# Performance work log

Hardware: AMD Instinct MI355X
Metric: run time of the kernel (lower is better)

The kernel has to match this reference:

```python
import jax, jax.numpy as jnp
import numpy as np

N = 50000          # num nodes
E = 800000         # num edges
DIN = 128          # in_channels
C = 64             # out_channels per head
H = 2              # heads
ED = 32            # edge_dim


def setup_inputs() -> dict:
    key = jax.random.key(0)
    ks = jax.random.split(key, 12)
    s = 1.0 / np.sqrt(DIN)
    se = 1.0 / np.sqrt(ED)
    return {
        "x": jax.random.normal(ks[0], (N, DIN), dtype=jnp.float32),
        "edge_index": jax.random.randint(ks[1], (2, E), 0, N, dtype=jnp.int32),
        "edge_attr": jax.random.normal(ks[2], (E, ED), dtype=jnp.float32),
        "Wq": jax.random.uniform(ks[3], (DIN, H * C), jnp.float32, -s, s),
        "bq": jax.random.uniform(ks[4], (H * C,), jnp.float32, -s, s),
        "Wk": jax.random.uniform(ks[5], (DIN, H * C), jnp.float32, -s, s),
        "bk": jax.random.uniform(ks[6], (H * C,), jnp.float32, -s, s),
        "Wv": jax.random.uniform(ks[7], (DIN, H * C), jnp.float32, -s, s),
        "bv": jax.random.uniform(ks[8], (H * C,), jnp.float32, -s, s),
        "We": jax.random.uniform(ks[9], (ED, H * C), jnp.float32, -se, se),
        "Wskip": jax.random.uniform(ks[10], (DIN, H * C), jnp.float32, -s, s),
        "bskip": jax.random.uniform(ks[11], (H * C,), jnp.float32, -s, s),
    }


def reference(x, edge_index, edge_attr, Wq, bq, Wk, bk, Wv, bv, We, Wskip, bskip):
    src, dst = edge_index[0], edge_index[1]
    # node-level projections [N, H, C]
    q = (x @ Wq + bq).reshape(N, H, C)
    k = (x @ Wk + bk).reshape(N, H, C)
    v = (x @ Wv + bv).reshape(N, H, C)
    e = (edge_attr @ We).reshape(E, H, C)  # lin_edge, no bias

    # per-edge gather
    q_e = q[dst]              # [E, H, C]
    k_e = k[src] + e          # key gets edge features
    alpha = jnp.einsum("ehc,ehc->eh", q_e, k_e) / jnp.sqrt(jnp.float32(C))

    # segment softmax over incoming edges of each dst node
    m = jax.ops.segment_max(alpha, dst, num_segments=N)       # [N, H]
    alpha = jnp.exp(alpha - m[dst])
    denom = jax.ops.segment_sum(alpha, dst, num_segments=N)   # [N, H]
    alpha = alpha / (denom[dst] + 1e-16)

    # weighted aggregation of values (value also gets edge features)
    msg = (v[src] + e) * alpha[..., None]                     # [E, H, C]
    out = jax.ops.segment_sum(msg, dst, num_segments=N)       # [N, H, C]
    out = out.reshape(N, H * C)

    # root weight skip connection (concat=True, beta=False)
    return out + x @ Wskip + bskip
```

## Files before the change

### kernel.cpp

```cpp
#include <hip/hip_runtime.h>
#include <cstdint>

#define NN 50000
#define EE 800000
#define DINC 128
#define HC 128
#define EDC 32
#define CAP 64
#define GEMM_BLKS 3128
#define SCAT_BLKS 3125
#define NB_SCAN 196

typedef __attribute__((ext_vector_type(8))) short short8;
typedef __attribute__((ext_vector_type(4))) float floatx4;

__device__ __forceinline__ unsigned int pk2(float a, float b){
  unsigned int ua = __float_as_uint(a), ub = __float_as_uint(b);
  ua = (ua + 0x7FFFu + ((ua >> 16) & 1u)) >> 16;
  ub = (ub + 0x7FFFu + ((ub >> 16) & 1u)) & 0xFFFF0000u;
  return ua | ub;
}
__device__ __forceinline__ float bflo(unsigned int p){ return __uint_as_float(p << 16); }
__device__ __forceinline__ float bfhi(unsigned int p){ return __uint_as_float(p & 0xFFFF0000u); }

__global__ __launch_bounds__(256) void k_fused(
    const float* __restrict__ x,
    const float* __restrict__ Wq, const float* __restrict__ bq,
    const float* __restrict__ Wk, const float* __restrict__ bk,
    const float* __restrict__ Wv, const float* __restrict__ bv,
    const float* __restrict__ Wsk, const float* __restrict__ bsk,
    const int* __restrict__ ei,
    unsigned int* __restrict__ qbf, unsigned int* __restrict__ kv,
    float* __restrict__ out, int* __restrict__ cnt, int2* __restrict__ eidsrc,
    const int do_scatter)
{
  __shared__ unsigned int smem[64*68 + 128*68];

  if (do_scatter && blockIdx.x >= GEMM_BLKS){
    int e = (blockIdx.x - GEMM_BLKS)*256 + threadIdx.x;
    if (e < EE){
      int d = ei[EE + e];
      int s = ei[e];
      int pos = atomicAdd(cnt + d, 1);
      if (pos < CAP) eidsrc[(size_t)d*CAP + pos] = make_int2(e, s);
    }
    return;
  }

  unsigned int* sx = smem;
  unsigned int* sw = smem + 64*68;
  float* facc = (float*)sw;

  const int tid = threadIdx.x;
  const int mat = blockIdx.x & 3;
  const int bm  = (blockIdx.x >> 2) * 64;
  const float* W  = (mat==0)?Wq:(mat==1)?Wk:(mat==2)?Wv:Wsk;
  const float* bi = (mat==0)?bq:(mat==1)?bk:(mat==2)?bv:bsk;

  for (int idx = tid; idx < 64*64; idx += 256){
    int row = idx >> 6, kk = idx & 63;
    int gr = bm + row;
    unsigned int p = 0u;
    if (gr < NN){
      float2 v = *(const float2*)(x + (size_t)gr*DINC + 2*kk);
      p = pk2(v.x, v.y);
    }
    sx[row*68 + kk] = p;
  }
  for (int idx = tid; idx < 64*64; idx += 256){
    int kp = idx >> 6;
    int n2 = (idx & 63) * 2;
    float2 a = *(const float2*)(W + (2*kp)*HC + n2);
    float2 b = *(const float2*)(W + (2*kp+1)*HC + n2);
    sw[n2*68 + kp]     = pk2(a.x, b.x);
    sw[(n2+1)*68 + kp] = pk2(a.y, b.y);
  }
  __syncthreads();

  const int l = tid & 63, wid = tid >> 6;
  const int lm = l & 15, ks = l >> 4;
  const int n0 = wid * 32;

  floatx4 acc[4][2];
  #pragma unroll
  for (int mt=0;mt<4;mt++) for(int nt=0;nt<2;nt++) acc[mt][nt] = (floatx4){0.f,0.f,0.f,0.f};

  #pragma unroll
  for (int kb = 0; kb < 4; ++kb){
    short8 a[4], b[2];
    #pragma unroll
    for (int mt=0;mt<4;mt++)
      a[mt] = *(const short8*)(sx + (mt*16+lm)*68 + kb*16 + ks*4);
    #pragma unroll
    for (int nt=0;nt<2;nt++)
      b[nt] = *(const short8*)(sw + (n0+nt*16+lm)*68 + kb*16 + ks*4);
    #pragma unroll
    for (int mt=0;mt<4;mt++)
      #pragma unroll
      for (int nt=0;nt<2;nt++)
        acc[mt][nt] = __builtin_amdgcn_mfma_f32_16x16x32_bf16(a[mt], b[nt], acc[mt][nt], 0, 0, 0);
  }
  __syncthreads();

  #pragma unroll
  for (int mt=0;mt<4;mt++)
    #pragma unroll
    for (int nt=0;nt<2;nt++)
      #pragma unroll
      for (int r=0;r<4;r++){
        int row = mt*16 + ks*4 + r;
        int col = n0 + nt*16 + lm;
        facc[row*132 + col] = acc[mt][nt][r];
      }
  __syncthreads();

  for (int idx = tid; idx < 64*64; idx += 256){
    int row = idx >> 6, cp = idx & 63;
    int gr = bm + row;
    if (gr >= NN) continue;
    float v0 = facc[row*132 + 2*cp]     + bi[2*cp];
    float v1 = facc[row*132 + 2*cp + 1] + bi[2*cp+1];
    if (mat == 0)      qbf[gr*64 + cp] = pk2(v0, v1);
    else if (mat == 1) kv[(size_t)gr*128 + 2*cp]     = pk2(v0, v1);
    else if (mat == 2) kv[(size_t)gr*128 + 2*cp + 1] = pk2(v0, v1);
    else *(float2*)(out + (size_t)gr*HC + 2*cp) = make_float2(v0, v1);
  }
}

__global__ __launch_bounds__(256) void k_count(const int* __restrict__ ei,
    int* __restrict__ cnt)
{
  int e = blockIdx.x*256 + threadIdx.x;
  if (e < EE) atomicAdd(cnt + ei[EE + e], 1);
}
__global__ __launch_bounds__(256) void k_blksum(const int* __restrict__ cnt,
    int* __restrict__ bsum)
{
  __shared__ int s[256];
  int t = threadIdx.x, i = blockIdx.x*256 + t;
  s[t] = (i < NN) ? cnt[i] : 0;
  __syncthreads();
  for (int d = 128; d > 0; d >>= 1){
    if (t < d) s[t] += s[t + d];
    __syncthreads();
  }
  if (t == 0) bsum[blockIdx.x] = s[0];
}
__global__ __launch_bounds__(256) void k_bscan(const int* __restrict__ bsum,
    int* __restrict__ bpre)
{
  __shared__ int s[256];
  int t = threadIdx.x;
  int v = (t < NB_SCAN) ? bsum[t] : 0;
  s[t] = v;
  __syncthreads();
  for (int d = 1; d < 256; d <<= 1){
    int u = (t >= d) ? s[t - d] : 0;
    __syncthreads();
    s[t] += u;
    __syncthreads();
  }
  if (t < NB_SCAN) bpre[t] = s[t] - v;
}
__global__ __launch_bounds__(256) void k_scan3(const int* __restrict__ cnt,
    const int* __restrict__ bpre, int* __restrict__ off, int* __restrict__ woff)
{
  __shared__ int s[256];
  int t = threadIdx.x, i = blockIdx.x*256 + t;
  int v = (i < NN) ? cnt[i] : 0;
  s[t] = v;
  __syncthreads();
  for (int d = 1; d < 256; d <<= 1){
    int u = (t >= d) ? s[t - d] : 0;
    __syncthreads();
    s[t] += u;
    __syncthreads();
  }
  if (i < NN){
    int o = bpre[blockIdx.x] + s[t] - v;
    off[i] = o; woff[i] = o;
  }
}
__global__ __launch_bounds__(256) void k_scatter(const int* __restrict__ ei,
    int* __restrict__ woff, int2* __restrict__ eidsrc)
{
  int e = blockIdx.x*256 + threadIdx.x;
  if (e < EE){
    int d = ei[EE + e];
    int s = ei[e];
    int pos = atomicAdd(woff + d, 1);
    eidsrc[pos] = make_int2(e, s);
  }
}

__global__ __launch_bounds__(256) void k_agg(
    const float* __restrict__ eattr, const float* __restrict__ We,
    const unsigned int* __restrict__ qbf, const uint2* __restrict__ kv,
    const int* __restrict__ cnt, const int* __restrict__ off,
    const int2* __restrict__ eidsrc, const int fixed,
    float* __restrict__ out)
{
  __shared__ float sWeT[128*33];
  const int tid = threadIdx.x;
  for (int idx = tid; idx < EDC*HC; idx += 256){
    int jj = idx >> 7, col = idx & 127;
    sWeT[col*33 + jj] = We[idx];
  }
  __syncthreads();

  const int wid = tid >> 6, l = tid & 63;
  const int node = blockIdx.x*4 + wid;
  const int h = l >> 5, j = l & 31;

  int deg = cnt[node]; if (deg > CAP) deg = CAP;
  const size_t beg = fixed ? (size_t)node*CAP : (size_t)off[node];
  int2 esl = eidsrc[beg + (fixed ? l : (l < deg ? l : 0))];

  unsigned int qp = qbf[node*64 + l];
  float q0 = bflo(qp), q1 = bfhi(qp);
  float Pl = 0.f;
  {
    const unsigned int* qrow = qbf + node*64 + h*32;
    const float* wt = sWeT + (h*64)*33 + j;
    #pragma unroll 8
    for (int cc = 0; cc < 32; ++cc){
      unsigned int up = qrow[cc];
      Pl += bflo(up)*wt[(2*cc)*33] + bfhi(up)*wt[(2*cc+1)*33];
    }
  }

  float acc0=0.f, acc1=0.f, wea=0.f, den=0.f;
  if (deg > 0){
    float eav[4]; uint2 kx[4];
    #pragma unroll
    for (int t = 0; t < 4; ++t){
      int it  = (t < deg) ? t : 0;
      int eid = __shfl(esl.x, it, 64);
      int src = __shfl(esl.y, it, 64);
      eav[t] = eattr[(size_t)eid*EDC + j];
      kx[t]  = kv[(size_t)src*64 + l];
    }
    for (int i = 0; i < deg; i += 4){
      float eavn[4]; uint2 kxn[4];
      const int inext = i + 4;
      if (inext < deg){
        #pragma unroll
        for (int t = 0; t < 4; ++t){
          int it  = (inext + t < deg) ? inext + t : inext;
          int eid = __shfl(esl.x, it, 64);
          int src = __shfl(esl.y, it, 64);
          eavn[t] = eattr[(size_t)eid*EDC + j];
          kxn[t]  = kv[(size_t)src*64 + l];
        }
      }
      float p[4];
      #pragma unroll
      for (int t = 0; t < 4; ++t)
        p[t] = q0*bflo(kx[t].x) + q1*bfhi(kx[t].x) + Pl*eav[t];
      #pragma unroll
      for (int s = 1; s < 32; s <<= 1){
        #pragma unroll
        for (int t = 0; t < 4; ++t) p[t] += __shfl_xor(p[t], s, 32);
      }
      const int nb = deg - i;
      #pragma unroll
      for (int t = 0; t < 4; ++t){
        float a = __expf(p[t] * 0.125f);
        if (t > 0) a = (t < nb) ? a : 0.f;
        den  += a;
        acc0 += a*bflo(kx[t].y);
        acc1 += a*bfhi(kx[t].y);
        wea  += a*eav[t];
      }
      #pragma unroll
      for (int t = 0; t < 4; ++t){ eav[t] = eavn[t]; kx[t] = kxn[t]; }
    }
  }

  float rden = 1.0f/(den + 1e-16f);
  float e0 = 0.f, e1 = 0.f;
  const float* w0 = sWeT + (2*l)*33;
  const float* w1 = sWeT + (2*l+1)*33;
  #pragma unroll 8
  for (int jj = 0; jj < 32; ++jj){
    float w = __shfl(wea, h*32 + jj, 64);
    e0 += w*w0[jj]; e1 += w*w1[jj];
  }
  float2 sk = *(const float2*)(out + (size_t)node*HC + 2*l);
  float2 o;
  o.x = sk.x + (acc0 + e0)*rden;
  o.y = sk.y + (acc1 + e1)*rden;
  *(float2*)(out + (size_t)node*HC + 2*l) = o;
}

extern "C" void kernel_launch(void* const* d_in, const int* in_sizes, int n_in,
                              void* d_out, int out_size, void* d_ws, size_t ws_size,
                              hipStream_t stream)
{
  const float* x   = (const float*)d_in[0];
  const int*   ei  = (const int*)d_in[1];
  const float* ea  = (const float*)d_in[2];
  const float* Wq  = (const float*)d_in[3];
  const float* bq  = (const float*)d_in[4];
  const float* Wk  = (const float*)d_in[5];
  const float* bk  = (const float*)d_in[6];
  const float* Wv  = (const float*)d_in[7];
  const float* bv  = (const float*)d_in[8];
  const float* We  = (const float*)d_in[9];
  const float* Wsk = (const float*)d_in[10];
  const float* bsk = (const float*)d_in[11];
  float* out = (float*)d_out;

  char* ws = (char*)d_ws;
  unsigned int* qbf = (unsigned int*)(ws);
  unsigned int* kvu = (unsigned int*)(ws + 12800000);
  int* cnt = (int*)(ws + 38400000);

  hipMemsetAsync(cnt, 0, NN*sizeof(int), stream);

  if (ws_size >= 64300000ull){
    int2* eidsrc = (int2*)(ws + 38600000);
    k_fused<<<GEMM_BLKS + SCAT_BLKS, 256, 0, stream>>>(
        x, Wq,bq, Wk,bk, Wv,bv, Wsk,bsk, ei, qbf, kvu, out, cnt, eidsrc, 1);
    k_agg<<<12500, 256, 0, stream>>>(ea, We, qbf, (const uint2*)kvu,
                                     cnt, (const int*)nullptr, eidsrc, 1, out);
  } else {
    int* off  = (int*)(ws + 38600000);
    int* woff = (int*)(ws + 38800000);
    int* bsum = (int*)(ws + 39000000);
    int* bpre = (int*)(ws + 39001024);
    int2* eidsrc = (int2*)(ws + 39002048);
    k_fused<<<GEMM_BLKS, 256, 0, stream>>>(
        x, Wq,bq, Wk,bk, Wv,bv, Wsk,bsk, ei, qbf, kvu, out, cnt, nullptr, 0);
    k_count  <<<SCAT_BLKS, 256, 0, stream>>>(ei, cnt);
    k_blksum <<<NB_SCAN, 256, 0, stream>>>(cnt, bsum);
    k_bscan  <<<1, 256, 0, stream>>>(bsum, bpre);
    k_scan3  <<<NB_SCAN, 256, 0, stream>>>(cnt, bpre, off, woff);
    k_scatter<<<SCAT_BLKS, 256, 0, stream>>>(ei, woff, eidsrc);
    k_agg<<<12500, 256, 0, stream>>>(ea, We, qbf, (const uint2*)kvu,
                                     cnt, off, eidsrc, 0, out);
  }
}
```

Measured before the change: 416.8 us.

## Process two nodes per wavefront in aggregation with wider per-lane loads

```diff
diff --git a/kernel.cpp b/kernel.cpp
--- a/kernel.cpp
+++ b/kernel.cpp
@@ -195,102 +195,116 @@
 
 __global__ __launch_bounds__(256) void k_agg(
     const float* __restrict__ eattr, const float* __restrict__ We,
-    const unsigned int* __restrict__ qbf, const uint2* __restrict__ kv,
+    const unsigned int* __restrict__ qbf, const unsigned int* __restrict__ kv,
     const int* __restrict__ cnt, const int* __restrict__ off,
     const int2* __restrict__ eidsrc, const int fixed,
     float* __restrict__ out)
 {
-  __shared__ float sWeT[128*33];
+  __shared__ unsigned int sWeTp[64*34];
+  __shared__ unsigned int sWe2p[32*64];
+  __shared__ float swea[8*64];
+
   const int tid = threadIdx.x;
-  for (int idx = tid; idx < EDC*HC; idx += 256){
+  for (int idx = tid; idx < 2048; idx += 256){
     int jj = idx >> 7, col = idx & 127;
-    sWeT[col*33 + jj] = We[idx];
+    sWeTp[(col & 63)*34 + (col >> 6)*17 + jj] =
+        pk2(We[(2*jj)*HC + col], We[(2*jj+1)*HC + col]);
+  }
+  for (int idx = tid; idx < 2048; idx += 256){
+    int j = idx >> 6, cp = idx & 63;
+    sWe2p[j*64 + cp] = pk2(We[j*HC + 2*cp], We[j*HC + 2*cp + 1]);
   }
   __syncthreads();
 
   const int wid = tid >> 6, l = tid & 63;
-  const int node = blockIdx.x*4 + wid;
-  const int h = l >> 5, j = l & 31;
-
-  int deg = cnt[node]; if (deg > CAP) deg = CAP;
+  const int half = l >> 5, m = l & 31;
+  const int h = m >> 4, mm = m & 15;
+  const int node = blockIdx.x*8 + wid*2 + half;
+
+  int deg = cnt[node];
+  if (fixed && deg > CAP) deg = CAP;
   const size_t beg = fixed ? (size_t)node*CAP : (size_t)off[node];
-  int2 esl = eidsrc[beg + (fixed ? l : (l < deg ? l : 0))];
-
-  unsigned int qp = qbf[node*64 + l];
-  float q0 = bflo(qp), q1 = bfhi(qp);
-  float Pl = 0.f;
+  const int dm1 = (deg > 0) ? deg - 1 : 0;
+  int degO = __shfl_xor(deg, 32, 64);
+  const int dmax = deg > degO ? deg : degO;
+
+  uint2 qp = *(const uint2*)(qbf + node*64 + h*32 + 2*mm);
+  float q0 = bflo(qp.x), q1 = bfhi(qp.x), q2 = bflo(qp.y), q3 = bfhi(qp.y);
+
+  float P2x = 0.f, P2y = 0.f;
   {
     const unsigned int* qrow = qbf + node*64 + h*32;
-    const float* wt = sWeT + (h*64)*33 + j;
+    const unsigned int* wt = sWeTp + h*17 + mm;
     #pragma unroll 8
     for (int cc = 0; cc < 32; ++cc){
       unsigned int up = qrow[cc];
-      Pl += bflo(up)*wt[(2*cc)*33] + bfhi(up)*wt[(2*cc+1)*33];
-    }
-  }
-
-  float acc0=0.f, acc1=0.f, wea=0.f, den=0.f;
-  if (deg > 0){
-    float eav[4]; uint2 kx[4];
+      unsigned int u0 = wt[(2*cc)*34];
+      unsigned int u1 = wt[(2*cc+1)*34];
+      P2x += bflo(up)*bflo(u0) + bfhi(up)*bflo(u1);
+      P2y += bflo(up)*bfhi(u0) + bfhi(up)*bfhi(u1);
+    }
+  }
+
+  float a0=0.f, a1=0.f, a2=0.f, a3=0.f;
+  float wx=0.f, wy=0.f, den=0.f;
+
+  for (int i = 0; i < dmax; i += 4){
+    int2 es[4]; float2 ea[4]; uint4 kx[4];
     #pragma unroll
     for (int t = 0; t < 4; ++t){
-      int it  = (t < deg) ? t : 0;
-      int eid = __shfl(esl.x, it, 64);
-      int src = __shfl(esl.y, it, 64);
-      eav[t] = eattr[(size_t)eid*EDC + j];
-      kx[t]  = kv[(size_t)src*64 + l];
-    }
-    for (int i = 0; i < deg; i += 4){
-      float eavn[4]; uint2 kxn[4];
-      const int inext = i + 4;
-      if (inext < deg){
-        #pragma unroll
-        for (int t = 0; t < 4; ++t){
-          int it  = (inext + t < deg) ? inext + t : inext;
-          int eid = __shfl(esl.x, it, 64);
-          int src = __shfl(esl.y, it, 64);
-          eavn[t] = eattr[(size_t)eid*EDC + j];
-          kxn[t]  = kv[(size_t)src*64 + l];
-        }
-      }
-      float p[4];
+      int it = i + t; it = it < dm1 ? it : dm1;
+      es[t] = eidsrc[beg + it];
+    }
+    #pragma unroll
+    for (int t = 0; t < 4; ++t){
+      int eid = min(max(es[t].x, 0), EE-1);
+      int src = min(max(es[t].y, 0), NN-1);
+      ea[t] = *(const float2*)(eattr + (size_t)eid*EDC + 2*mm);
+      kx[t] = *(const uint4*)(kv + (size_t)src*128 + h*64 + 4*mm);
+    }
+    float p[4];
+    #pragma unroll
+    for (int t = 0; t < 4; ++t)
+      p[t] = q0*bflo(kx[t].x) + q1*bfhi(kx[t].x)
+           + q2*bflo(kx[t].z) + q3*bfhi(kx[t].z)
+           + P2x*ea[t].x + P2y*ea[t].y;
+    #pragma unroll
+    for (int s = 1; s < 16; s <<= 1){
       #pragma unroll
-      for (int t = 0; t < 4; ++t)
-        p[t] = q0*bflo(kx[t].x) + q1*bfhi(kx[t].x) + Pl*eav[t];
-      #pragma unroll
-      for (int s = 1; s < 32; s <<= 1){
-        #pragma unroll
-        for (int t = 0; t < 4; ++t) p[t] += __shfl_xor(p[t], s, 32);
-      }
-      const int nb = deg - i;
-      #pragma unroll
-      for (int t = 0; t < 4; ++t){
-        float a = __expf(p[t] * 0.125f);
-        if (t > 0) a = (t < nb) ? a : 0.f;
-        den  += a;
-        acc0 += a*bflo(kx[t].y);
-        acc1 += a*bfhi(kx[t].y);
-        wea  += a*eav[t];
-      }
-      #pragma unroll
-      for (int t = 0; t < 4; ++t){ eav[t] = eavn[t]; kx[t] = kxn[t]; }
-    }
-  }
-
+      for (int t = 0; t < 4; ++t) p[t] += __shfl_xor(p[t], s, 64);
+    }
+    #pragma unroll
+    for (int t = 0; t < 4; ++t){
+      float al = ((i + t) < deg) ? __expf(p[t]*0.125f) : 0.f;
+      den += al;
+      a0 += al*bflo(kx[t].y); a1 += al*bfhi(kx[t].y);
+      a2 += al*bflo(kx[t].w); a3 += al*bfhi(kx[t].w);
+      wx += al*ea[t].x;       wy += al*ea[t].y;
+    }
+  }
+
+  const int slot = wid*2 + half;
+  *(float2*)(swea + slot*64 + h*32 + 2*mm) = make_float2(wx, wy);
+  float e0=0.f, e1=0.f, e2=0.f, e3=0.f;
+  {
+    const float* sv = swea + slot*64 + h*32;
+    const unsigned int* w2 = sWe2p + h*32 + 2*mm;
+    #pragma unroll 8
+    for (int j = 0; j < 32; ++j){
+      float w = sv[j];
+      uint2 u = *(const uint2*)(w2 + j*64);
+      e0 += w*bflo(u.x); e1 += w*bfhi(u.x);
+      e2 += w*bflo(u.y); e3 += w*bfhi(u.y);
+    }
+  }
   float rden = 1.0f/(den + 1e-16f);
-  float e0 = 0.f, e1 = 0.f;
-  const float* w0 = sWeT + (2*l)*33;
-  const float* w1 = sWeT + (2*l+1)*33;
-  #pragma unroll 8
-  for (int jj = 0; jj < 32; ++jj){
-    float w = __shfl(wea, h*32 + jj, 64);
-    e0 += w*w0[jj]; e1 += w*w1[jj];
-  }
-  float2 sk = *(const float2*)(out + (size_t)node*HC + 2*l);
-  float2 o;
-  o.x = sk.x + (acc0 + e0)*rden;
-  o.y = sk.y + (acc1 + e1)*rden;
-  *(float2*)(out + (size_t)node*HC + 2*l) = o;
+  float4 sk = *(const float4*)(out + (size_t)node*HC + h*64 + 4*mm);
+  float4 o;
+  o.x = sk.x + (a0 + e0)*rden;
+  o.y = sk.y + (a1 + e1)*rden;
+  o.z = sk.z + (a2 + e2)*rden;
+  o.w = sk.w + (a3 + e3)*rden;
+  *(float4*)(out + (size_t)node*HC + h*64 + 4*mm) = o;
 }
 
 extern "C" void kernel_launch(void* const* d_in, const int* in_sizes, int n_in,
@@ -322,8 +336,8 @@
     int2* eidsrc = (int2*)(ws + 38600000);
     k_fused<<<GEMM_BLKS + SCAT_BLKS, 256, 0, stream>>>(
         x, Wq,bq, Wk,bk, Wv,bv, Wsk,bsk, ei, qbf, kvu, out, cnt, eidsrc, 1);
-    k_agg<<<12500, 256, 0, stream>>>(ea, We, qbf, (const uint2*)kvu,
-                                     cnt, (const int*)nullptr, eidsrc, 1, out);
+    k_agg<<<6250, 256, 0, stream>>>(ea, We, qbf, kvu,
+                                    cnt, (const int*)nullptr, eidsrc, 1, out);
   } else {
     int* off  = (int*)(ws + 38600000);
     int* woff = (int*)(ws + 38800000);
@@ -337,7 +351,7 @@
     k_bscan  <<<1, 256, 0, stream>>>(bsum, bpre);
     k_scan3  <<<NB_SCAN, 256, 0, stream>>>(cnt, bpre, off, woff);
     k_scatter<<<SCAT_BLKS, 256, 0, stream>>>(ei, woff, eidsrc);
-    k_agg<<<12500, 256, 0, stream>>>(ea, We, qbf, (const uint2*)kvu,
-                                     cnt, off, eidsrc, 0, out);
-  }
-}
+    k_agg<<<6250, 256, 0, stream>>>(ea, We, qbf, kvu,
+                                    cnt, off, eidsrc, 0, out);
+  }
+}
```

After: 435.6 us. +4.5%, slower.
